# Kernel tuning notes

Measured on AMD Instinct MI355X. Metric: run time of the kernel, lower is better.

The kernel has to match this reference:

```python
import jax, jax.numpy as jnp
import numpy as np
from jax import lax

D_MODEL = 1024
D_STATE = 16
D_CONV = 4
EXPAND = 2
D_INNER = EXPAND * D_MODEL          # 2048
DT_RANK = (D_MODEL + 15) // 16       # 64
BATCH, SEQLEN = 2, 2048


def setup_inputs() -> dict:
    key = jax.random.key(0)
    ks = jax.random.split(key, 12)
    s = 0.02
    inp = {
        "hidden_states": jax.random.normal(ks[0], (BATCH, SEQLEN, D_MODEL), jnp.float32),
        "ln_w": jnp.ones((D_MODEL,), jnp.float32),
        "ln_b": jnp.zeros((D_MODEL,), jnp.float32),
        "in_proj_w": jax.random.normal(ks[1], (2 * D_INNER, D_MODEL), jnp.float32) * s,
        "conv_w": jax.random.normal(ks[2], (D_INNER, D_CONV), jnp.float32) * s,
        "conv_b": jnp.zeros((D_INNER,), jnp.float32),
        "x_proj_w": jax.random.normal(ks[3], (DT_RANK + 2 * D_STATE, D_INNER), jnp.float32) * s,
        "dt_proj_w": jax.random.normal(ks[4], (D_INNER, DT_RANK), jnp.float32) * s,
        "dt_proj_b": jax.random.uniform(ks[5], (D_INNER,), jnp.float32, -4.0, -2.0),
        "A_log": jnp.log(jnp.broadcast_to(jnp.arange(1, D_STATE + 1, dtype=jnp.float32), (D_INNER, D_STATE))),
        "D_param": jnp.ones((D_INNER,), jnp.float32),
        "out_proj_w": jax.random.normal(ks[6], (D_MODEL, D_INNER), jnp.float32) * s,
    }
    return inp


def _layernorm(x, w, b, eps=1e-5):
    mu = jnp.mean(x, axis=-1, keepdims=True)
    var = jnp.mean(jnp.square(x - mu), axis=-1, keepdims=True)
    return (x - mu) * lax.rsqrt(var + eps) * w + b


def _mamba_forward(x_in, in_proj_w, conv_w, conv_b, x_proj_w, dt_proj_w,
                   dt_proj_b, A_log, D_param, out_proj_w):
    B, L, _ = x_in.shape
    xz = x_in @ in_proj_w.T                      # (B, L, 2*ED)
    x, z = jnp.split(xz, 2, axis=-1)             # each (B, L, ED)

    # depthwise causal conv along time
    xt = x.transpose(0, 2, 1)                    # (B, ED, L)
    xc = lax.conv_general_dilated(
        xt, conv_w[:, None, :],                  # kernel (ED, 1, K)
        window_strides=(1,), padding=[(D_CONV - 1, 0)],
        dimension_numbers=("NCH", "OIH", "NCH"),
        feature_group_count=D_INNER)
    x = jax.nn.silu((xc + conv_b[None, :, None]).transpose(0, 2, 1))  # (B, L, ED)

    x_dbl = x @ x_proj_w.T                       # (B, L, R + 2N)
    dt, Bc, Cc = jnp.split(x_dbl, [DT_RANK, DT_RANK + D_STATE], axis=-1)
    dt = jax.nn.softplus(dt @ dt_proj_w.T + dt_proj_b)   # (B, L, ED)

    A = -jnp.exp(A_log)                          # (ED, N)

    def step(h, inp):
        dt_t, x_t, B_t, C_t = inp                # (B,ED),(B,ED),(B,N),(B,N)
        dA = jnp.exp(dt_t[..., None] * A)        # (B, ED, N)
        dBx = (dt_t * x_t)[..., None] * B_t[:, None, :]
        h = dA * h + dBx
        y = jnp.einsum("ben,bn->be", h, C_t)
        return h, y

    h0 = jnp.zeros((B, D_INNER, D_STATE), x.dtype)
    xs = (dt.transpose(1, 0, 2), x.transpose(1, 0, 2),
          Bc.transpose(1, 0, 2), Cc.transpose(1, 0, 2))
    _, ys = lax.scan(step, h0, xs)               # ys: (L, B, ED)
    y = ys.transpose(1, 0, 2) + x * D_param
    y = y * jax.nn.silu(z)
    return y @ out_proj_w.T                      # (B, L, d_model)


def reference(hidden_states, ln_w, ln_b, in_proj_w, conv_w, conv_b,
              x_proj_w, dt_proj_w, dt_proj_b, A_log, D_param, out_proj_w):
    residual = hidden_states
    h = _layernorm(hidden_states, ln_w, ln_b)
    h = _mamba_forward(h, in_proj_w, conv_w, conv_b, x_proj_w,
                       dt_proj_w, dt_proj_b, A_log, D_param, out_proj_w)
    return residual + h
```

## Files before the change

kernel.cpp:

```cpp
#include <hip/hip_runtime.h>

#define DM 1024
#define ED 2048
#define LEN 2048
#define NB 2
#define NROWS (NB*LEN)
#define DTR 64
#define NST 16
#define XDBL 96
#define NCH 64
#define CHL 32
#define LOG2E 1.44269504f

typedef __attribute__((ext_vector_type(8))) __bf16 bf16x8;
typedef __attribute__((ext_vector_type(8))) short short8;
typedef __attribute__((ext_vector_type(4))) float f32x4;
typedef unsigned short u16;
typedef unsigned int u32;
typedef __attribute__((ext_vector_type(4))) unsigned short u16x4;

__device__ __forceinline__ u16 f2bf(float f){
  union { float f; unsigned int u; } v; v.f = f;
  unsigned int u = v.u;
  return (u16)((u + 0x7FFFu + ((u >> 16) & 1u)) >> 16);
}
__device__ __forceinline__ float bf2f(u16 h){
  union { unsigned int u; float f; } v; v.u = ((unsigned int)h) << 16; return v.f;
}

__device__ __forceinline__ void gload16(const u16* g, u16* l){
  __builtin_amdgcn_global_load_lds((const __attribute__((address_space(1))) unsigned int*)(g),
                                   (__attribute__((address_space(3))) unsigned int*)(l), 16, 0, 0);
}

__global__ __launch_bounds__(256) void k_cvt_all(
    const float* __restrict__ w0, const float* __restrict__ w1,
    const float* __restrict__ w2, const float* __restrict__ w3,
    u16* __restrict__ o0, u16* __restrict__ o1, u16* __restrict__ o2, u16* __restrict__ o3){
  int i = blockIdx.x*256 + threadIdx.x;
  const int n0 = 4194304/4, n1 = 196608/4, n2 = 131072/4, n3 = 2097152/4;
  const float* src; u16* dst; int off;
  if (i < n0){ src=w0; dst=o0; off=i; }
  else if (i < n0+n1){ src=w1; dst=o1; off=i-n0; }
  else if (i < n0+n1+n2){ src=w2; dst=o2; off=i-n0-n1; }
  else if (i < n0+n1+n2+n3){ src=w3; dst=o3; off=i-n0-n1-n2; }
  else return;
  float4 v = reinterpret_cast<const float4*>(src)[off];
  u16x4 o; o[0]=f2bf(v.x); o[1]=f2bf(v.y); o[2]=f2bf(v.z); o[3]=f2bf(v.w);
  reinterpret_cast<u16x4*>(dst)[off] = o;
}

__global__ __launch_bounds__(256) void k_ln(const float* __restrict__ x, const float* __restrict__ w,
                                            const float* __restrict__ b, u16* __restrict__ out){
  int row = blockIdx.x;
  const float4* xp = reinterpret_cast<const float4*>(x + (size_t)row*DM);
  float4 v = xp[threadIdx.x];
  float s  = v.x+v.y+v.z+v.w;
  float sq = v.x*v.x+v.y*v.y+v.z*v.z+v.w*v.w;
  #pragma unroll
  for (int off=32; off; off>>=1){ s += __shfl_xor(s, off); sq += __shfl_xor(sq, off); }
  __shared__ float red[8];
  int wid = threadIdx.x>>6, lane = threadIdx.x&63;
  if (!lane){ red[wid]=s; red[4+wid]=sq; }
  __syncthreads();
  s  = red[0]+red[1]+red[2]+red[3];
  sq = red[4]+red[5]+red[6]+red[7];
  float mean = s * (1.0f/DM);
  float var  = sq * (1.0f/DM) - mean*mean;
  float rstd = rsqrtf(var + 1e-5f);
  int c0 = threadIdx.x*4;
  float vals[4] = {v.x,v.y,v.z,v.w};
  u16x4 o;
  #pragma unroll
  for (int j=0;j<4;j++){
    int c = c0+j;
    o[j] = f2bf((vals[j]-mean)*rstd*w[c] + b[c]);
  }
  *reinterpret_cast<u16x4*>(out + (size_t)row*DM + c0) = o;
}

template<int WM, int WN, int MFR, int NFR, int EPI, int OUTBF>
__global__ __launch_bounds__(WM*WN*64, 2) void k_gemm8p(
    const u16* __restrict__ A, const u16* __restrict__ B,
    void* __restrict__ Cv, int K, int lda, int ldb, int ldc,
    const float* __restrict__ res)
{
  constexpr int THREADS = WM*WN*64;
  constexpr int BM = WM*MFR*16, BN = WN*NFR*16;
  constexpr int MH = MFR/2;
  static_assert(BM*4/THREADS == 2 && BN*4/THREADS == 2, "2 loads per half-tile per thread");
  __shared__ u16 Asl[2][2][BM*32];
  __shared__ u16 Bsl[2][2][BN*32];
  int t    = threadIdx.x;
  int lane = t & 63;
  int w    = t >> 6;
  int wr = w / WN, wc = w % WN;
  int nwg = gridDim.x*gridDim.y;
  int bid = blockIdx.y*gridDim.x + blockIdx.x;
  int swz = (bid & 7)*(nwg >> 3) + (bid >> 3);
  int bn_i = swz % gridDim.y, bm_i = swz / gridDim.y;
  int bm = bm_i*BM, bn = bn_i*BN;
  int r  = lane & 15;
  int slotz = (((lane >> 4) ^ ((r >> 1) & 3))) * 8;

  const u16* Ag = A + (size_t)bm*lda;
  const u16* Bg = B + (size_t)bn*ldb;

  f32x4 acc[MFR][NFR];
  #pragma unroll
  for (int i=0;i<MFR;i++)
    #pragma unroll
    for (int j=0;j<NFR;j++) acc[i][j] = (f32x4)0.f;

  auto stageA = [&](int buf, int kh, int kt){
    #pragma unroll
    for (int j=0;j<2;j++){
      int p  = (j*THREADS + t)*16;
      int pl = p ^ (((p>>7)&3)<<4);
      gload16(Ag + (size_t)(pl>>6)*lda + kt*64 + kh*32 + ((pl&63)>>1), &Asl[buf][kh][p>>1]);
    }
  };
  auto stageB = [&](int buf, int kh, int kt){
    #pragma unroll
    for (int j=0;j<2;j++){
      int p  = (j*THREADS + t)*16;
      int pl = p ^ (((p>>7)&3)<<4);
      gload16(Bg + (size_t)(pl>>6)*ldb + kt*64 + kh*32 + ((pl&63)>>1), &Bsl[buf][kh][p>>1]);
    }
  };
  auto ldsA = [&](int buf, int kh, int mh, short8* a){
    const u16* Ar = &Asl[buf][kh][(wr*(MFR*16) + mh*(MH*16) + r)*32 + slotz];
    #pragma unroll
    for (int i=0;i<MH;i++) a[i] = *reinterpret_cast<const short8*>(Ar + i*16*32);
  };
  auto ldsB = [&](int buf, int kh, short8* b){
    const u16* Br = &Bsl[buf][kh][(wc*(NFR*16) + r)*32 + slotz];
    #pragma unroll
    for (int j=0;j<NFR;j++) b[j] = *reinterpret_cast<const short8*>(Br + j*16*32);
  };
  auto mmacL = [&](short8* a, short8* b){
    __builtin_amdgcn_s_setprio(1);
    #pragma unroll
    for (int i=0;i<MH;i++)
      #pragma unroll
      for (int j=0;j<NFR;j++)
        acc[i][j] = __builtin_amdgcn_mfma_f32_16x16x32_bf16(
            __builtin_bit_cast(bf16x8, a[i]), __builtin_bit_cast(bf16x8, b[j]), acc[i][j], 0,0,0);
    __builtin_amdgcn_s_setprio(0);
  };
  auto mmacH = [&](short8* a, short8* b){
    __builtin_amdgcn_s_setprio(1);
    #pragma unroll
    for (int i=0;i<MH;i++)
      #pragma unroll
      for (int j=0;j<NFR;j++)
        acc[MH+i][j] = __builtin_amdgcn_mfma_f32_16x16x32_bf16(
            __builtin_bit_cast(bf16x8, a[i]), __builtin_bit_cast(bf16x8, b[j]), acc[MH+i][j], 0,0,0);
    __builtin_amdgcn_s_setprio(0);
  };

  const int NT = K >> 6;
  stageA(0,0,0); stageB(0,0,0); stageA(0,1,0); stageB(0,1,0);
  asm volatile("s_waitcnt vmcnt(4)" ::: "memory");
  __builtin_amdgcn_s_barrier();
  __builtin_amdgcn_sched_barrier(0);

  int cur = 0;
  for (int tau=0; tau<NT; ++tau){
    int nxt = cur^1;
    int sx  = (tau+1 < NT) ? tau+1 : 0;
    short8 a0[MH], b0[NFR];
    ldsA(cur, 0, 0, a0);
    ldsB(cur, 0, b0);
    stageA(nxt, 0, sx);
    __builtin_amdgcn_s_barrier();
    asm volatile("s_waitcnt lgkmcnt(0)" ::: "memory");
    __builtin_amdgcn_sched_barrier(0);
    mmacL(a0, b0);
    __builtin_amdgcn_s_barrier();
    short8 a1[MH];
    ldsA(cur, 0, 1, a1);
    stageB(nxt, 0, sx);
    __builtin_amdgcn_s_barrier();
    asm volatile("s_waitcnt lgkmcnt(0)" ::: "memory");
    __builtin_amdgcn_sched_barrier(0);
    mmacH(a1, b0);
    asm volatile("s_waitcnt vmcnt(4)" ::: "memory");
    __builtin_amdgcn_s_barrier();
    short8 a2[MH], b1[NFR];
    ldsA(cur, 1, 0, a2);
    ldsB(cur, 1, b1);
    stageA(nxt, 1, sx);
    __builtin_amdgcn_s_barrier();
    asm volatile("s_waitcnt lgkmcnt(0)" ::: "memory");
    __builtin_amdgcn_sched_barrier(0);
    mmacL(a2, b1);
    __builtin_amdgcn_s_barrier();
    short8 a3[MH];
    ldsA(cur, 1, 1, a3);
    stageB(nxt, 1, sx);
    __builtin_amdgcn_s_barrier();
    asm volatile("s_waitcnt lgkmcnt(0)" ::: "memory");
    __builtin_amdgcn_sched_barrier(0);
    mmacH(a3, b1);
    asm volatile("s_waitcnt vmcnt(4)" ::: "memory");
    __builtin_amdgcn_s_barrier();
    cur = nxt;
  }

  int rowbase = bm + wr*(MFR*16) + (lane>>4)*4;
  int colbase = bn + wc*(NFR*16) + (lane&15);
  float* Cf = (float*)Cv;
  u16*   Cb = (u16*)Cv;
  #pragma unroll
  for (int mi=0;mi<MFR;mi++){
    #pragma unroll
    for (int j=0;j<NFR;j++){
      #pragma unroll
      for (int tt=0;tt<4;tt++){
        int m = rowbase + mi*16 + tt;
        int n = colbase + j*16;
        float v = acc[mi][j][tt];
        if (EPI==2){ v += res[(size_t)m*ldc + n]; }
        if (OUTBF) Cb[(size_t)m*ldc + n] = f2bf(v);
        else       Cf[(size_t)m*ldc + n] = v;
      }
    }
  }
}

template<int WM, int WN, int MREP, int NREP>
__global__ __launch_bounds__(WM*WN*64) void k_gemm_dsk(
    const u16* __restrict__ A, const u16* __restrict__ B,
    u16* __restrict__ P, int Kh, int lda, int ldb, int ldc, size_t Msz)
{
  constexpr int THREADS = WM*WN*64;
  constexpr int BM = WM*MREP*16, BN = WN*NREP*16;
  constexpr int AL = BM*4/THREADS;
  constexpr int BL = BN*4/THREADS;
  __shared__ u16 As[3][BM*32];
  __shared__ u16 Bs[3][BN*32];
  int t    = threadIdx.x;
  int lane = t & 63;
  int w    = t >> 6;
  int wm = w % WM, wn = w / WM;
  int gx = gridDim.x, gy = gridDim.y;
  int total = gx*gy*2;
  int lin = blockIdx.x + blockIdx.y*gx + blockIdx.z*gx*gy;
  int swz = (lin & 7)*(total >> 3) + (lin >> 3);
  int bn_i = swz % gy;
  int kz   = (swz / gy) & 1;
  int bm_i = swz / (gy*2);
  int bm = bm_i*BM, bn = bn_i*BN;
  int r  = lane & 15;
  int ks = (lane >> 4) * 8;
  int ksz = ks ^ (((r>>1)&3)<<3);

  const u16* Ab = A + (size_t)bm*lda + kz*Kh;
  const u16* Bb = B + (size_t)bn*ldb + kz*Kh;
  u16* Cp = P + kz*Msz;

  f32x4 acc[MREP][NREP];
  #pragma unroll
  for (int i=0;i<MREP;i++)
    #pragma unroll
    for (int j=0;j<NREP;j++) acc[i][j] = (f32x4)0.f;

  auto stage = [&](int buf, int kk){
    #pragma unroll
    for (int j=0;j<AL;j++){
      int p  = (j*THREADS + t)*16;
      int pl = p ^ (((p>>7)&3)<<4);
      gload16(Ab + (size_t)(pl>>6)*lda + kk + ((pl&63)>>1), &As[buf][p>>1]);
    }
    #pragma unroll
    for (int j=0;j<BL;j++){
      int p  = (j*THREADS + t)*16;
      int pl = p ^ (((p>>7)&3)<<4);
      gload16(Bb + (size_t)(pl>>6)*ldb + kk + ((pl&63)>>1), &Bs[buf][p>>1]);
    }
  };

  auto compute = [&](int buf){
    const u16* Ar = &As[buf][(wm*MREP*16 + r)*32 + ksz];
    const u16* Br = &Bs[buf][(wn*NREP*16 + r)*32 + ksz];
    short8 a[MREP], b[NREP];
    #pragma unroll
    for (int i=0;i<MREP;i++) a[i] = *reinterpret_cast<const short8*>(Ar + i*16*32);
    #pragma unroll
    for (int j=0;j<NREP;j++) b[j] = *reinterpret_cast<const short8*>(Br + j*16*32);
    __builtin_amdgcn_s_setprio(1);
    #pragma unroll
    for (int i=0;i<MREP;i++)
      #pragma unroll
      for (int j=0;j<NREP;j++)
        acc[i][j] = __builtin_amdgcn_mfma_f32_16x16x32_bf16(
            __builtin_bit_cast(bf16x8, a[i]), __builtin_bit_cast(bf16x8, b[j]), acc[i][j], 0,0,0);
    __builtin_amdgcn_s_setprio(0);
  };

  const int NT = Kh >> 5;
  stage(0, 0);
  stage(1, 32);
  asm volatile("s_waitcnt vmcnt(4)" ::: "memory");
  __builtin_amdgcn_s_barrier();
  __builtin_amdgcn_sched_barrier(0);

  int bufc = 0;
  for (int tt=0; tt<NT; ++tt){
    int nx = tt + 2; if (nx >= NT) nx -= NT;
    int bufn = bufc + 2; if (bufn >= 3) bufn -= 3;
    stage(bufn, nx*32);
    compute(bufc);
    asm volatile("s_waitcnt vmcnt(4)" ::: "memory");
    __builtin_amdgcn_s_barrier();
    __builtin_amdgcn_sched_barrier(0);
    if (++bufc == 3) bufc = 0;
  }

  int rowbase = bm + wm*(MREP*16) + (lane>>4)*4;
  int colbase = bn + wn*(NREP*16) + (lane&15);
  #pragma unroll
  for (int i=0;i<MREP;i++)
    #pragma unroll
    for (int j=0;j<NREP;j++)
      #pragma unroll
      for (int tt=0;tt<4;tt++)
        Cp[(size_t)(rowbase + i*16 + tt)*ldc + colbase + j*16] = f2bf(acc[i][j][tt]);
}

__global__ __launch_bounds__(256) void k_fin(const u16* __restrict__ p0, const u16* __restrict__ p1,
                                             const float* __restrict__ res, float* __restrict__ out){
  int i = blockIdx.x*256 + threadIdx.x;
  u16x4 a = reinterpret_cast<const u16x4*>(p0)[i];
  u16x4 b = reinterpret_cast<const u16x4*>(p1)[i];
  float4 c = reinterpret_cast<const float4*>(res)[i];
  float4 o;
  o.x = bf2f(a[0]) + bf2f(b[0]) + c.x;
  o.y = bf2f(a[1]) + bf2f(b[1]) + c.y;
  o.z = bf2f(a[2]) + bf2f(b[2]) + c.z;
  o.w = bf2f(a[3]) + bf2f(b[3]) + c.w;
  reinterpret_cast<float4*>(out)[i] = o;
}

template<int MI, int NI, int EPI, int OUTBF>
__global__ __launch_bounds__(256) void k_gemm128(
    const u16* __restrict__ A, const u16* __restrict__ B,
    void* __restrict__ Cv, int K, int lda, int ldb, int ldc,
    const float* __restrict__ bias, const float* __restrict__ res)
{
  constexpr int AISS = MI/2, BISS = NI/2;
  __shared__ u16 As[2][32*MI*32];
  __shared__ u16 Bs[2][32*NI*32];
  int t    = threadIdx.x;
  int lane = t & 63;
  int w    = t >> 6;
  int wm = w & 1, wn = w >> 1;
  int bm = blockIdx.x * (32*MI), bn = blockIdx.y * (32*NI);
  int r  = lane & 15;
  int ks = (lane >> 4) * 8;
  int ksz = ks ^ (((r>>1)&3)<<3);

  const u16* Ab = A + (size_t)bm*lda;
  const u16* Bb = B + (size_t)bn*ldb;

  f32x4 acc[MI][NI];
  #pragma unroll
  for (int i=0;i<MI;i++)
    #pragma unroll
    for (int j=0;j<NI;j++) acc[i][j] = (f32x4)0.f;

  auto stage = [&](int buf, int kk){
    #pragma unroll
    for (int j=0;j<AISS;j++){
      int p  = (j*256 + t)*16;
      int pl = p ^ (((p>>7)&3)<<4);
      gload16(Ab + (size_t)(pl>>6)*lda + kk + ((pl&63)>>1), &As[buf][p>>1]);
    }
    #pragma unroll
    for (int j=0;j<BISS;j++){
      int p  = (j*256 + t)*16;
      int pl = p ^ (((p>>7)&3)<<4);
      gload16(Bb + (size_t)(pl>>6)*ldb + kk + ((pl&63)>>1), &Bs[buf][p>>1]);
    }
  };

  auto compute = [&](int buf){
    const u16* Ar = &As[buf][(wm*(MI*16) + r)*32 + ksz];
    const u16* Br = &Bs[buf][(wn*(NI*16) + r)*32 + ksz];
    short8 a[MI], b[NI];
    #pragma unroll
    for (int i=0;i<MI;i++) a[i] = *reinterpret_cast<const short8*>(Ar + i*16*32);
    #pragma unroll
    for (int j=0;j<NI;j++) b[j] = *reinterpret_cast<const short8*>(Br + j*16*32);
    #pragma unroll
    for (int i=0;i<MI;i++)
      #pragma unroll
      for (int j=0;j<NI;j++)
        acc[i][j] = __builtin_amdgcn_mfma_f32_16x16x32_bf16(
            __builtin_bit_cast(bf16x8, a[i]), __builtin_bit_cast(bf16x8, b[j]), acc[i][j], 0,0,0);
  };

  stage(0, 0);
  __syncthreads();
  int cur = 0;
  for (int kk=32; kk<K; kk+=32){
    stage(cur^1, kk);
    compute(cur);
    __syncthreads();
    cur ^= 1;
  }
  compute(cur);

  int rowbase = bm + wm*(MI*16) + (lane>>4)*4;
  int colbase = bn + wn*(NI*16) + (lane&15);
  float* Cf = (float*)Cv;
  u16*   Cb = (u16*)Cv;
  #pragma unroll
  for (int i=0;i<MI;i++){
    #pragma unroll
    for (int j=0;j<NI;j++){
      #pragma unroll
      for (int tt=0;tt<4;tt++){
        int m = rowbase + i*16 + tt;
        int n = colbase + j*16;
        float v = acc[i][j][tt];
        if (EPI==1){ v += bias[n]; v = (v > 20.f) ? v : __logf(1.f + __expf(v)); }
        if (EPI==2){ v += res[(size_t)m*ldc + n]; }
        if (OUTBF) Cb[(size_t)m*ldc + n] = f2bf(v);
        else       Cf[(size_t)m*ldc + n] = v;
      }
    }
  }
}

__global__ __launch_bounds__(512) void k_gemm_xp(
    const u16* __restrict__ A, const u16* __restrict__ B, u16* __restrict__ C)
{
  __shared__ float red[8][16][97];
  int t = threadIdx.x;
  int lane = t & 63;
  int w = t >> 6;
  int bm = blockIdx.x * 16;
  int r  = lane & 15;
  int ks = (lane >> 4) * 8;
  int k0 = w * 256;
  const u16* Ap = A + (size_t)(bm + r)*2048 + k0 + ks;
  const u16* Bp = B + (size_t)r*2048 + k0 + ks;
  f32x4 acc[6];
  #pragma unroll
  for (int j=0;j<6;j++) acc[j] = (f32x4)0.f;
  #pragma unroll
  for (int kk=0; kk<256; kk+=32){
    short8 a = *reinterpret_cast<const short8*>(Ap + kk);
    #pragma unroll
    for (int j=0;j<6;j++){
      short8 b = *reinterpret_cast<const short8*>(Bp + (size_t)j*16*2048 + kk);
      acc[j] = __builtin_amdgcn_mfma_f32_16x16x32_bf16(
          __builtin_bit_cast(bf16x8, a), __builtin_bit_cast(bf16x8, b), acc[j], 0,0,0);
    }
  }
  #pragma unroll
  for (int j=0;j<6;j++)
    #pragma unroll
    for (int tt=0;tt<4;tt++)
      red[w][(lane>>4)*4+tt][(lane&15)+j*16] = acc[j][tt];
  __syncthreads();
  for (int o = t; o < 1536; o += 512){
    int rr = o / 96, cc = o % 96;
    float s = 0.f;
    #pragma unroll
    for (int ww=0; ww<8; ww++) s += red[ww][rr][cc];
    C[(size_t)(bm+rr)*96 + cc] = f2bf(s);
  }
}

__global__ __launch_bounds__(256) void k_conv(const u16* __restrict__ xz, const float* __restrict__ cw,
                                              const float* __restrict__ cb, u16* __restrict__ xc){
  int g = blockIdx.x*256 + threadIdx.x;
  int e  = g & (ED-1);
  int lg = g >> 11;
  int b  = lg >> 8;
  int l0 = (lg & 255) * 8;
  int row0 = b*LEN + l0;
  float w0=cw[e*4], w1=cw[e*4+1], w2=cw[e*4+2], w3=cw[e*4+3];
  float cbe = cb[e];
  float xv[11];
  #pragma unroll
  for (int i=0;i<11;i++){
    int l = l0 + i - 3;
    xv[i] = (l>=0) ? bf2f(xz[(size_t)(row0 + i - 3)*(2*ED) + e]) : 0.f;
  }
  #pragma unroll
  for (int s=0;s<8;s++){
    float acc = cbe + xv[s]*w0 + xv[s+1]*w1 + xv[s+2]*w2 + xv[s+3]*w3;
    float sv = acc / (1.f + __expf(-acc));
    xc[(size_t)(row0+s)*ED + e] = f2bf(sv);
  }
}

__global__ __launch_bounds__(256) void k_scan1(const u16* __restrict__ dt, const u16* __restrict__ xc,
    const u16* __restrict__ xdb, float* __restrict__ S, u16* __restrict__ Q)
{
  __shared__ float Bsl[CHL][NST];
  int bid = blockIdx.x;
  int eg = bid & 7;
  int ch = (bid >> 3) & (NCH-1);
  int b  = bid >> 9;
  int e  = eg*256 + threadIdx.x;
  int row0 = b*LEN + ch*CHL;

  for (int i = threadIdx.x; i < CHL*NST; i += 256){
    int rl = i >> 4, n = i & 15;
    Bsl[rl][n] = bf2f(xdb[(size_t)(row0+rl)*XDBL + DTR + n]);
  }
  __syncthreads();

  float h[NST];
  #pragma unroll
  for (int n=0;n<NST;n++) h[n]=0.f;
  float Ssum = 0.f;

  for (int s=0;s<CHL;s++){
    int row = row0 + s;
    float dtv = bf2f(dt[(size_t)row*ED + e]);
    float xv  = bf2f(xc[(size_t)row*ED + e]);
    Ssum += dtv;
    float dx = dtv*xv;
    float r = exp2f(-LOG2E*dtv);
    float bl[NST];
    #pragma unroll
    for (int q=0;q<4;q++){
      float4 v = *reinterpret_cast<const float4*>(&Bsl[s][q*4]);
      bl[q*4]=v.x; bl[q*4+1]=v.y; bl[q*4+2]=v.z; bl[q*4+3]=v.w;
    }
    float p = r;
    #pragma unroll
    for (int n=0;n<NST;n++){
      h[n] = p*h[n] + dx*bl[n];
      if (n<NST-1) p *= r;
    }
  }
  size_t base = (size_t)(b*NCH+ch)*NST*ED + e;
  #pragma unroll
  for (int n=0;n<NST;n++) Q[base + (size_t)n*ED] = f2bf(h[n]);
  S[(size_t)(b*NCH+ch)*ED + e] = Ssum;
}

__global__ __launch_bounds__(256) void k_scan2(const float* __restrict__ S, const u16* __restrict__ Q,
                                               u16* __restrict__ H){
  int idx = blockIdx.x*256 + threadIdx.x;
  int e = idx & (ED-1);
  int n = (idx >> 11) & (NST-1);
  int b = idx >> 15;
  float An = -(float)(n+1) * LOG2E;
  float h = 0.f;
  for (int c=0;c<NCH;c++){
    size_t qo = ((size_t)(b*NCH+c)*NST + n)*ED + e;
    H[qo] = f2bf(h);
    float sv = S[(size_t)(b*NCH+c)*ED + e];
    h = exp2f(An*sv)*h + bf2f(Q[qo]);
  }
}

__global__ __launch_bounds__(256) void k_scan3(const u16* __restrict__ dt, const u16* __restrict__ xc,
    const u16* __restrict__ xdb, const u16* __restrict__ H,
    const float* __restrict__ Dp, const u16* __restrict__ xz, u16* __restrict__ yb)
{
  __shared__ float Bsl[CHL][NST], Csl[CHL][NST];
  int bid = blockIdx.x;
  int eg = bid & 7;
  int ch = (bid >> 3) & (NCH-1);
  int b  = bid >> 9;
  int e  = eg*256 + threadIdx.x;
  int row0 = b*LEN + ch*CHL;

  for (int i = threadIdx.x; i < CHL*NST*2; i += 256){
    int rl = i >> 5, j = i & 31;
    float v = bf2f(xdb[(size_t)(row0+rl)*XDBL + DTR + j]);
    if (j < 16) Bsl[rl][j] = v;
    else        Csl[rl][j-16] = v;
  }
  __syncthreads();

  float h[NST];
  size_t hb = (size_t)(b*NCH+ch)*NST*ED + e;
  #pragma unroll
  for (int n=0;n<NST;n++) h[n] = bf2f(H[hb + (size_t)n*ED]);
  float dpe = Dp[e];

  for (int s=0;s<CHL;s++){
    int row = row0 + s;
    float dtv = bf2f(dt[(size_t)row*ED + e]);
    float xv  = bf2f(xc[(size_t)row*ED + e]);
    float dx = dtv*xv;
    float r = exp2f(-LOG2E*dtv);
    float bl[NST], cl[NST];
    #pragma unroll
    for (int q=0;q<4;q++){
      float4 v = *reinterpret_cast<const float4*>(&Bsl[s][q*4]);
      bl[q*4]=v.x; bl[q*4+1]=v.y; bl[q*4+2]=v.z; bl[q*4+3]=v.w;
      float4 u = *reinterpret_cast<const float4*>(&Csl[s][q*4]);
      cl[q*4]=u.x; cl[q*4+1]=u.y; cl[q*4+2]=u.z; cl[q*4+3]=u.w;
    }
    float p = r;
    float y = 0.f;
    #pragma unroll
    for (int n=0;n<NST;n++){
      h[n] = p*h[n] + dx*bl[n];
      y += h[n]*cl[n];
      if (n<NST-1) p *= r;
    }
    y += xv*dpe;
    float z = bf2f(xz[(size_t)row*(2*ED) + ED + e]);
    float sz = z / (1.f + __expf(-z));
    yb[(size_t)row*ED + e] = f2bf(y*sz);
  }
}

extern "C" void kernel_launch(void* const* d_in, const int* in_sizes, int n_in,
                              void* d_out, int out_size, void* d_ws, size_t ws_size,
                              hipStream_t stream) {
  const float* hid    = (const float*)d_in[0];
  const float* ln_w   = (const float*)d_in[1];
  const float* ln_b   = (const float*)d_in[2];
  const float* w_in   = (const float*)d_in[3];
  const float* conv_w = (const float*)d_in[4];
  const float* conv_b = (const float*)d_in[5];
  const float* w_xp   = (const float*)d_in[6];
  const float* w_dt   = (const float*)d_in[7];
  const float* dt_b   = (const float*)d_in[8];
  const float* Dp     = (const float*)d_in[10];
  const float* w_op   = (const float*)d_in[11];
  float* out = (float*)d_out;

  char* p = (char*)d_ws;
  auto alloc = [&](size_t bytes)->char* {
    char* q = p; p += (bytes + 255) & ~(size_t)255; return q;
  };
  u16*   w_in_b = (u16*)  alloc((size_t)4096*1024*2);
  u16*   w_xp_b = (u16*)  alloc((size_t)96*2048*2);
  u16*   w_dt_b = (u16*)  alloc((size_t)2048*64*2);
  u16*   w_op_b = (u16*)  alloc((size_t)1024*2048*2);
  u16*   h_ln   = (u16*)  alloc((size_t)NROWS*DM*2);
  u16*   xz     = (u16*)  alloc((size_t)NROWS*2*ED*2);
  u16*   xc     = (u16*)  alloc((size_t)NROWS*ED*2);
  u16*   xdbl_b = (u16*)  alloc((size_t)NROWS*XDBL*2);
  u16*   dtf    = (u16*)  alloc((size_t)NROWS*ED*2);
  float* S      = (float*)alloc((size_t)NB*NCH*ED*4);
  u16*   Q      = (u16*)  alloc((size_t)NB*NCH*ED*NST*2);
  u16*   H      = (u16*)  alloc((size_t)NB*NCH*ED*NST*2);
  u16*   yb     = (u16*)  alloc((size_t)NROWS*ED*2);

  k_cvt_all<<<(1654784+255)/256,256,0,stream>>>(w_in, w_xp, w_dt, w_op,
                                                w_in_b, w_xp_b, w_dt_b, w_op_b);

  k_ln<<<NROWS,256,0,stream>>>(hid, ln_w, ln_b, h_ln);

  dim3 g1(4096/256, 4096/256);
  k_gemm8p<2,4,8,4,0,1><<<g1,512,0,stream>>>(h_ln, w_in_b, xz, 1024, 1024, 1024, 4096, nullptr);

  k_conv<<<NROWS*ED/(256*8),256,0,stream>>>(xz, conv_w, conv_b, xc);

  k_gemm_xp<<<4096/16,512,0,stream>>>(xc, w_xp_b, xdbl_b);

  dim3 g3(4096/128, 2048/128);
  k_gemm128<4,4,1,1><<<g3,256,0,stream>>>(xdbl_b, w_dt_b, dtf, 64, 96, 64, 2048, dt_b, nullptr);

  k_scan1<<<NB*NCH*8,256,0,stream>>>(dtf, xc, xdbl_b, S, Q);
  k_scan2<<<256,256,0,stream>>>(S, Q, H);
  k_scan3<<<NB*NCH*8,256,0,stream>>>(dtf, xc, xdbl_b, H, Dp, xz, yb);

  dim3 g4(4096/128, 1024/128, 2);
  k_gemm_dsk<2,2,4,4><<<g4,256,0,stream>>>(yb, w_op_b, Q, 1024, 2048, 2048, 1024, (size_t)4096*1024);

  k_fin<<<(4096*1024/4)/256,256,0,stream>>>(Q, H, hid, out);
}
```

Before: 188.0 us.

## Fuse dt projection GEMM and softplus into both scan kernels

Removes the standalone dt_proj GEMM kernel and the materialized dt buffer (4096x2048 bf16). Each scan block now computes its own 32x256 dt tile with MFMA from the low-rank xdbl slice and dt weights, applies bias and softplus, and stores it in shared memory. This saves a kernel launch plus a round trip of dt through global memory, written once and read twice. The cost is doing the small K=64 GEMM twice (in scan1 and scan3) and extra shared memory per block.

```diff
diff --git a/kernel.cpp b/kernel.cpp
--- a/kernel.cpp
+++ b/kernel.cpp
@@ -343,97 +343,6 @@
   reinterpret_cast<float4*>(out)[i] = o;
 }
 
-template<int MI, int NI, int EPI, int OUTBF>
-__global__ __launch_bounds__(256) void k_gemm128(
-    const u16* __restrict__ A, const u16* __restrict__ B,
-    void* __restrict__ Cv, int K, int lda, int ldb, int ldc,
-    const float* __restrict__ bias, const float* __restrict__ res)
-{
-  constexpr int AISS = MI/2, BISS = NI/2;
-  __shared__ u16 As[2][32*MI*32];
-  __shared__ u16 Bs[2][32*NI*32];
-  int t    = threadIdx.x;
-  int lane = t & 63;
-  int w    = t >> 6;
-  int wm = w & 1, wn = w >> 1;
-  int bm = blockIdx.x * (32*MI), bn = blockIdx.y * (32*NI);
-  int r  = lane & 15;
-  int ks = (lane >> 4) * 8;
-  int ksz = ks ^ (((r>>1)&3)<<3);
-
-  const u16* Ab = A + (size_t)bm*lda;
-  const u16* Bb = B + (size_t)bn*ldb;
-
-  f32x4 acc[MI][NI];
-  #pragma unroll
-  for (int i=0;i<MI;i++)
-    #pragma unroll
-    for (int j=0;j<NI;j++) acc[i][j] = (f32x4)0.f;
-
-  auto stage = [&](int buf, int kk){
-    #pragma unroll
-    for (int j=0;j<AISS;j++){
-      int p  = (j*256 + t)*16;
-      int pl = p ^ (((p>>7)&3)<<4);
-      gload16(Ab + (size_t)(pl>>6)*lda + kk + ((pl&63)>>1), &As[buf][p>>1]);
-    }
-    #pragma unroll
-    for (int j=0;j<BISS;j++){
-      int p  = (j*256 + t)*16;
-      int pl = p ^ (((p>>7)&3)<<4);
-      gload16(Bb + (size_t)(pl>>6)*ldb + kk + ((pl&63)>>1), &Bs[buf][p>>1]);
-    }
-  };
-
-  auto compute = [&](int buf){
-    const u16* Ar = &As[buf][(wm*(MI*16) + r)*32 + ksz];
-    const u16* Br = &Bs[buf][(wn*(NI*16) + r)*32 + ksz];
-    short8 a[MI], b[NI];
-    #pragma unroll
-    for (int i=0;i<MI;i++) a[i] = *reinterpret_cast<const short8*>(Ar + i*16*32);
-    #pragma unroll
-    for (int j=0;j<NI;j++) b[j] = *reinterpret_cast<const short8*>(Br + j*16*32);
-    #pragma unroll
-    for (int i=0;i<MI;i++)
-      #pragma unroll
-      for (int j=0;j<NI;j++)
-        acc[i][j] = __builtin_amdgcn_mfma_f32_16x16x32_bf16(
-            __builtin_bit_cast(bf16x8, a[i]), __builtin_bit_cast(bf16x8, b[j]), acc[i][j], 0,0,0);
-  };
-
-  stage(0, 0);
-  __syncthreads();
-  int cur = 0;
-  for (int kk=32; kk<K; kk+=32){
-    stage(cur^1, kk);
-    compute(cur);
-    __syncthreads();
-    cur ^= 1;
-  }
-  compute(cur);
-
-  int rowbase = bm + wm*(MI*16) + (lane>>4)*4;
-  int colbase = bn + wn*(NI*16) + (lane&15);
-  float* Cf = (float*)Cv;
-  u16*   Cb = (u16*)Cv;
-  #pragma unroll
-  for (int i=0;i<MI;i++){
-    #pragma unroll
-    for (int j=0;j<NI;j++){
-      #pragma unroll
-      for (int tt=0;tt<4;tt++){
-        int m = rowbase + i*16 + tt;
-        int n = colbase + j*16;
-        float v = acc[i][j][tt];
-        if (EPI==1){ v += bias[n]; v = (v > 20.f) ? v : __logf(1.f + __expf(v)); }
-        if (EPI==2){ v += res[(size_t)m*ldc + n]; }
-        if (OUTBF) Cb[(size_t)m*ldc + n] = f2bf(v);
-        else       Cf[(size_t)m*ldc + n] = v;
-      }
-    }
-  }
-}
-
 __global__ __launch_bounds__(512) void k_gemm_xp(
     const u16* __restrict__ A, const u16* __restrict__ B, u16* __restrict__ C)
 {
@@ -499,10 +408,14 @@
   }
 }
 
-__global__ __launch_bounds__(256) void k_scan1(const u16* __restrict__ dt, const u16* __restrict__ xc,
-    const u16* __restrict__ xdb, float* __restrict__ S, u16* __restrict__ Q)
+
+__global__ __launch_bounds__(256) void k_scan1(const u16* __restrict__ xc,
+    const u16* __restrict__ xdb, const u16* __restrict__ w_dt, const float* __restrict__ dt_b,
+    float* __restrict__ S, u16* __restrict__ Q)
 {
   __shared__ float Bsl[CHL][NST];
+  __shared__ u16 Xs[CHL][80];
+  __shared__ u16 dts[CHL][264];
   int bid = blockIdx.x;
   int eg = bid & 7;
   int ch = (bid >> 3) & (NCH-1);
@@ -514,6 +427,52 @@
     int rl = i >> 4, n = i & 15;
     Bsl[rl][n] = bf2f(xdb[(size_t)(row0+rl)*XDBL + DTR + n]);
   }
+  {
+    int rl = threadIdx.x >> 3, c8 = (threadIdx.x & 7)*8;
+    *reinterpret_cast<short8*>(&Xs[rl][c8]) =
+        *reinterpret_cast<const short8*>(xdb + (size_t)(row0+rl)*XDBL + c8);
+  }
+  __syncthreads();
+
+  {
+    int lane = threadIdx.x & 63;
+    int wv   = threadIdx.x >> 6;
+    int r = lane & 15, kslot = lane >> 4;
+    f32x4 dacc[2][4];
+    #pragma unroll
+    for (int mt=0;mt<2;mt++)
+      #pragma unroll
+      for (int nt=0;nt<4;nt++) dacc[mt][nt] = (f32x4)0.f;
+    #pragma unroll
+    for (int kk=0;kk<2;kk++){
+      short8 af[2], bfr[4];
+      #pragma unroll
+      for (int mt=0;mt<2;mt++)
+        af[mt] = *reinterpret_cast<const short8*>(&Xs[mt*16 + r][kk*32 + kslot*8]);
+      #pragma unroll
+      for (int nt=0;nt<4;nt++)
+        bfr[nt] = *reinterpret_cast<const short8*>(w_dt + (size_t)(eg*256 + wv*64 + nt*16 + r)*DTR + kk*32 + kslot*8);
+      #pragma unroll
+      for (int mt=0;mt<2;mt++)
+        #pragma unroll
+        for (int nt=0;nt<4;nt++)
+          dacc[mt][nt] = __builtin_amdgcn_mfma_f32_16x16x32_bf16(
+              __builtin_bit_cast(bf16x8, af[mt]), __builtin_bit_cast(bf16x8, bfr[nt]), dacc[mt][nt], 0,0,0);
+    }
+    #pragma unroll
+    for (int mt=0;mt<2;mt++)
+      #pragma unroll
+      for (int nt=0;nt<4;nt++){
+        int cc = wv*64 + nt*16 + r;
+        float bia = dt_b[eg*256 + cc];
+        #pragma unroll
+        for (int tt=0;tt<4;tt++){
+          float v = dacc[mt][nt][tt] + bia;
+          v = (v > 20.f) ? v : __logf(1.f + __expf(v));
+          dts[mt*16 + kslot*4 + tt][cc] = f2bf(v);
+        }
+      }
+  }
   __syncthreads();
 
   float h[NST];
@@ -523,7 +482,7 @@
 
   for (int s=0;s<CHL;s++){
     int row = row0 + s;
-    float dtv = bf2f(dt[(size_t)row*ED + e]);
+    float dtv = bf2f(dts[s][threadIdx.x]);
     float xv  = bf2f(xc[(size_t)row*ED + e]);
     Ssum += dtv;
     float dx = dtv*xv;
@@ -563,11 +522,14 @@
   }
 }
 
-__global__ __launch_bounds__(256) void k_scan3(const u16* __restrict__ dt, const u16* __restrict__ xc,
-    const u16* __restrict__ xdb, const u16* __restrict__ H,
-    const float* __restrict__ Dp, const u16* __restrict__ xz, u16* __restrict__ yb)
+__global__ __launch_bounds__(256) void k_scan3(const u16* __restrict__ xc,
+    const u16* __restrict__ xdb, const u16* __restrict__ w_dt, const float* __restrict__ dt_b,
+    const u16* __restrict__ H, const float* __restrict__ Dp, const u16* __restrict__ xz,
+    u16* __restrict__ yb)
 {
   __shared__ float Bsl[CHL][NST], Csl[CHL][NST];
+  __shared__ u16 Xs[CHL][80];
+  __shared__ u16 dts[CHL][264];
   int bid = blockIdx.x;
   int eg = bid & 7;
   int ch = (bid >> 3) & (NCH-1);
@@ -581,6 +543,52 @@
     if (j < 16) Bsl[rl][j] = v;
     else        Csl[rl][j-16] = v;
   }
+  {
+    int rl = threadIdx.x >> 3, c8 = (threadIdx.x & 7)*8;
+    *reinterpret_cast<short8*>(&Xs[rl][c8]) =
+        *reinterpret_cast<const short8*>(xdb + (size_t)(row0+rl)*XDBL + c8);
+  }
+  __syncthreads();
+
+  {
+    int lane = threadIdx.x & 63;
+    int wv   = threadIdx.x >> 6;
+    int r = lane & 15, kslot = lane >> 4;
+    f32x4 dacc[2][4];
+    #pragma unroll
+    for (int mt=0;mt<2;mt++)
+      #pragma unroll
+      for (int nt=0;nt<4;nt++) dacc[mt][nt] = (f32x4)0.f;
+    #pragma unroll
+    for (int kk=0;kk<2;kk++){
+      short8 af[2], bfr[4];
+      #pragma unroll
+      for (int mt=0;mt<2;mt++)
+        af[mt] = *reinterpret_cast<const short8*>(&Xs[mt*16 + r][kk*32 + kslot*8]);
+      #pragma unroll
+      for (int nt=0;nt<4;nt++)
+        bfr[nt] = *reinterpret_cast<const short8*>(w_dt + (size_t)(eg*256 + wv*64 + nt*16 + r)*DTR + kk*32 + kslot*8);
+      #pragma unroll
+      for (int mt=0;mt<2;mt++)
+        #pragma unroll
+        for (int nt=0;nt<4;nt++)
+          dacc[mt][nt] = __builtin_amdgcn_mfma_f32_16x16x32_bf16(
+              __builtin_bit_cast(bf16x8, af[mt]), __builtin_bit_cast(bf16x8, bfr[nt]), dacc[mt][nt], 0,0,0);
+    }
+    #pragma unroll
+    for (int mt=0;mt<2;mt++)
+      #pragma unroll
+      for (int nt=0;nt<4;nt++){
+        int cc = wv*64 + nt*16 + r;
+        float bia = dt_b[eg*256 + cc];
+        #pragma unroll
+        for (int tt=0;tt<4;tt++){
+          float v = dacc[mt][nt][tt] + bia;
+          v = (v > 20.f) ? v : __logf(1.f + __expf(v));
+          dts[mt*16 + kslot*4 + tt][cc] = f2bf(v);
+        }
+      }
+  }
   __syncthreads();
 
   float h[NST];
@@ -591,7 +599,7 @@
 
   for (int s=0;s<CHL;s++){
     int row = row0 + s;
-    float dtv = bf2f(dt[(size_t)row*ED + e]);
+    float dtv = bf2f(dts[s][threadIdx.x]);
     float xv  = bf2f(xc[(size_t)row*ED + e]);
     float dx = dtv*xv;
     float r = exp2f(-LOG2E*dtv);
@@ -646,7 +654,6 @@
   u16*   xz     = (u16*)  alloc((size_t)NROWS*2*ED*2);
   u16*   xc     = (u16*)  alloc((size_t)NROWS*ED*2);
   u16*   xdbl_b = (u16*)  alloc((size_t)NROWS*XDBL*2);
-  u16*   dtf    = (u16*)  alloc((size_t)NROWS*ED*2);
   float* S      = (float*)alloc((size_t)NB*NCH*ED*4);
   u16*   Q      = (u16*)  alloc((size_t)NB*NCH*ED*NST*2);
   u16*   H      = (u16*)  alloc((size_t)NB*NCH*ED*NST*2);
@@ -664,12 +671,9 @@
 
   k_gemm_xp<<<4096/16,512,0,stream>>>(xc, w_xp_b, xdbl_b);
 
-  dim3 g3(4096/128, 2048/128);
-  k_gemm128<4,4,1,1><<<g3,256,0,stream>>>(xdbl_b, w_dt_b, dtf, 64, 96, 64, 2048, dt_b, nullptr);
-
-  k_scan1<<<NB*NCH*8,256,0,stream>>>(dtf, xc, xdbl_b, S, Q);
+  k_scan1<<<NB*NCH*8,256,0,stream>>>(xc, xdbl_b, w_dt_b, dt_b, S, Q);
   k_scan2<<<256,256,0,stream>>>(S, Q, H);
-  k_scan3<<<NB*NCH*8,256,0,stream>>>(dtf, xc, xdbl_b, H, Dp, xz, yb);
+  k_scan3<<<NB*NCH*8,256,0,stream>>>(xc, xdbl_b, w_dt_b, dt_b, H, Dp, xz, yb);
 
   dim3 g4(4096/128, 1024/128, 2);
   k_gemm_dsk<2,2,4,4><<<g4,256,0,stream>>>(yb, w_op_b, Q, 1024, 2048, 2048, 1024, (size_t)4096*1024);
```

Result: no change. 187.9 us (-0.0%).
